# Kernel optimization log

Measured on AMD Instinct MI355X. Metric: run time of the kernel, lower is better.

## Reference

```python
import jax, jax.numpy as jnp
import numpy as np

# ---- static config (mirrors init_kwargs) ----
IN_CH = 64; COND_CH = 80; STRIDE = 8
DILATIONS = (1, 3, 9, 27); KS = 3; HOP = 256
HID = 64; KPKS = 3
B = 4; IN_LEN = 4096; COND_LEN = 128
N_LAYERS = len(DILATIONS)
OUT_CH = 2 * IN_CH
LW = IN_CH * OUT_CH * KS * N_LAYERS  # 98304
LB = OUT_CH * N_LAYERS               # 512


def leaky(x):
    return jax.nn.leaky_relu(x, 0.2)


def conv1d(x, w, b, dilation=1):
    # x: (B, T, Cin), w: (K, Cin, Cout) -> (B, T, Cout), 'same' padding
    y = jax.lax.conv_general_dilated(x, w, (1,), 'SAME', rhs_dilation=(dilation,),
                                     dimension_numbers=('NWC', 'WIO', 'NWC'))
    return y + b


def lvc(x, kernel, bias, hop):
    """Location-variable convolution, faithful to the TF extract_patches/reflect-pad
    implementation (call site uses dilation=1, kernel_size=3).
    x: (B, T, Cin); kernel: (B, L, Cin, Cout, K); bias: (B, L, Cout); T == L*hop."""
    Bn, T, C = x.shape
    K = kernel.shape[-1]
    p = (K - 1) // 2  # dilation = 1
    xp = jnp.pad(x, ((0, 0), (p, p), (0, 0)))
    L = T // hop
    # im2col: overlapping hop-segments of length hop+2p, stride hop -> (B, L, hop+2p, C)
    idx = jnp.arange(L)[:, None] * hop + jnp.arange(hop + 2 * p)[None, :]
    patches = xp[:, idx, :]
    patches = jnp.swapaxes(patches, 2, 3)  # (B, L, C, hop+2p)
    pad2 = hop - 1  # hop_size - dilation
    patches = jnp.pad(patches, ((0, 0), (0, 0), (0, 0), (pad2, pad2)), mode='reflect')
    patches = patches.reshape(Bn, L, C, -1, K)  # (B, L, C, hop, K) since 3*hop == hop*K
    out = jnp.einsum('blisk,bliok->blso', patches, kernel)  # (B, L, hop, Cout)
    out = out + bias[:, :, None, :]
    return out.reshape(Bn, T, -1)


def setup_inputs() -> dict:
    key = jax.random.key(0)
    ks = jax.random.split(key, 16)

    def w(k, shape):
        fan_in = float(np.prod(shape[:-1]))
        return (jax.random.normal(k, shape) / np.sqrt(fan_in)).astype(jnp.float32)

    return {
        'x': jax.random.normal(ks[0], (B, IN_LEN, IN_CH), jnp.float32),
        'c': jax.random.normal(ks[1], (B, COND_LEN, COND_CH), jnp.float32),
        # convt_pre transposed conv: (K=2*stride, Cin, Cout)
        'ct_w': w(ks[2], (2 * STRIDE, IN_CH, IN_CH)),
        'ct_b': jnp.zeros((IN_CH,), jnp.float32),
        # per-layer dilated convs (stacked over layers)
        'conv_w': w(ks[3], (N_LAYERS, KS, IN_CH, IN_CH)),
        'conv_b': jnp.zeros((N_LAYERS, IN_CH), jnp.float32),
        # kernel predictor: input conv
        'inp_w': w(ks[4], (5, COND_CH, HID)),
        'inp_b': jnp.zeros((HID,), jnp.float32),
        # 3 residual blocks, each with two convs
        'res_w1': w(ks[5], (3, KPKS, HID, HID)),
        'res_b1': jnp.zeros((3, HID), jnp.float32),
        'res_w2': w(ks[6], (3, KPKS, HID, HID)),
        'res_b2': jnp.zeros((3, HID), jnp.float32),
        # kernel / bias heads
        'kern_w': w(ks[7], (KPKS, HID, LW)),
        'kern_b': jnp.zeros((LW,), jnp.float32),
        'bias_w': w(ks[8], (KPKS, HID, LB)),
        'bias_b': jnp.zeros((LB,), jnp.float32),
    }


def reference(x, c, ct_w, ct_b, conv_w, conv_b, inp_w, inp_b,
              res_w1, res_b1, res_w2, res_b2, kern_w, kern_b, bias_w, bias_b):
    Bn = x.shape[0]
    # ---- convt_pre: LeakyReLU + ConvTranspose1d(stride, kernel=2*stride, 'same') ----
    h = leaky(x)
    h = jax.lax.conv_transpose(h, ct_w, strides=(STRIDE,), padding='SAME',
                               dimension_numbers=('NWC', 'WIO', 'NWC')) + ct_b
    # h: (B, IN_LEN*STRIDE, IN_CH)

    # ---- kernel predictor ----
    cc = leaky(conv1d(c, inp_w, inp_b))
    for j in range(3):
        t = leaky(conv1d(cc, res_w1[j], res_b1[j]))
        t = leaky(conv1d(t, res_w2[j], res_b2[j]))
        cc = cc + t
    k = conv1d(cc, kern_w, kern_b)   # (B, COND_LEN, LW)
    bb = conv1d(cc, bias_w, bias_b)  # (B, COND_LEN, LB)
    # faithful to TF: reshape (B, COND_LEN, LW) row-major into (B, layers, COND_LEN, ...)
    kernels = k.reshape(Bn, N_LAYERS, COND_LEN, IN_CH, OUT_CH, KS)
    biases = bb.reshape(Bn, N_LAYERS, COND_LEN, OUT_CH)

    # ---- LVC layers with sigmoid-tanh gating ----
    for i, d in enumerate(DILATIONS):
        out = leaky(conv1d(leaky(h), conv_w[i], conv_b[i], dilation=d))
        out = lvc(out, kernels[:, i], biases[:, i], HOP)  # (B, T, 2*IN_CH)
        h = h + jax.nn.sigmoid(out[..., :IN_CH]) * jnp.tanh(out[..., IN_CH:])
    return h
```

## Files before the change

### kernel.cpp

```cpp
#include <hip/hip_runtime.h>

#define TSZ 32768
#define LWN 98304

typedef float f32x4 __attribute__((ext_vector_type(4)));
typedef float f32x8 __attribute__((ext_vector_type(8)));
typedef short s16x8 __attribute__((ext_vector_type(8)));
typedef unsigned short u16x8 __attribute__((ext_vector_type(8)));

__device__ __forceinline__ float leaky(float x) { return x > 0.f ? x : 0.2f * x; }
__device__ __forceinline__ float bf2f(unsigned short b) { return __uint_as_float(((unsigned)b) << 16); }
__device__ __forceinline__ unsigned short f2bf(float f) {
  unsigned u = __float_as_uint(f);
  u += 0x7fffu + ((u >> 16) & 1u);
  return (unsigned short)(u >> 16);
}

__global__ __launch_bounds__(256) void ct_kernel(const float* __restrict__ x,
                                                 const float* __restrict__ ct_w,
                                                 const float* __restrict__ ct_b,
                                                 float* __restrict__ h) {
  __shared__ float wl[2 * 64 * 64];
  __shared__ float xl[17 * 64];
  int bid = blockIdx.x;
  int qc = bid & 255, phi = (bid >> 8) & 7, b = bid >> 11;
  int w0 = (11 - phi) & 7;
  int d0 = (phi + w0 - 11) >> 3;
  int tid = threadIdx.x;
  for (int e = tid; e < 8192; e += 256) {
    int w2 = e >> 12, rest = e & 4095;
    wl[e] = ct_w[(w0 + 8 * w2) * 4096 + rest];
  }
  int mstart = qc * 16 + d0;
  for (int e = tid; e < 17 * 64; e += 256) {
    int mr = e >> 6, i = e & 63;
    int m = mstart + mr;
    xl[e] = (m >= 0 && m < 4096) ? leaky(x[((b << 12) + m) * 64 + i]) : 0.f;
  }
  __syncthreads();
  int o = tid & 63, tg4 = tid >> 6;
  float bv = ct_b[o];
  float acc[4] = {bv, bv, bv, bv};
  for (int w2 = 0; w2 < 2; w2++) {
    const float* wp = &wl[w2 * 4096];
    int rbase = tg4 * 4 + w2;
    const float* xp = &xl[rbase * 64];
    for (int i = 0; i < 64; i++) {
      float wv = wp[i * 64 + o];
      acc[0] += xp[i] * wv;
      acc[1] += xp[64 + i] * wv;
      acc[2] += xp[128 + i] * wv;
      acc[3] += xp[192 + i] * wv;
    }
  }
  for (int r = 0; r < 4; r++) {
    int t = (qc * 16 + tg4 * 4 + r) * 8 + phi;
    h[(((size_t)b << 15) + t) * 64 + o] = acc[r];
  }
}

__global__ __launch_bounds__(256) void conv5_kernel(const float* __restrict__ c,
                                                    const float* __restrict__ w,
                                                    const float* __restrict__ bias,
                                                    float* __restrict__ cc) {
  int f = blockIdx.x * 256 + threadIdx.x;
  int o = f & 63, t = (f >> 6) & 127, b = f >> 13;
  float acc = bias[o];
  for (int kk = 0; kk < 5; kk++) {
    int tt = t + kk - 2;
    if (tt < 0 || tt >= 128) continue;
    const float* cr = c + (b * 128 + tt) * 80;
    const float* wr = w + kk * 80 * 64 + o;
    for (int i = 0; i < 80; i++) acc += cr[i] * wr[i * 64];
  }
  cc[f] = leaky(acc);
}

template <int ADD>
__global__ __launch_bounds__(256) void conv3_kernel(const float* __restrict__ xin,
                                                    const float* __restrict__ w,
                                                    const float* __restrict__ bias,
                                                    const float* __restrict__ addsrc,
                                                    float* __restrict__ out) {
  int f = blockIdx.x * 256 + threadIdx.x;
  int o = f & 63, t = (f >> 6) & 127, b = f >> 13;
  float acc = bias[o];
  for (int kk = 0; kk < 3; kk++) {
    int tt = t + kk - 1;
    if (tt < 0 || tt >= 128) continue;
    const float* xr = xin + (b * 128 + tt) * 64;
    const float* wr = w + kk * 64 * 64 + o;
    for (int i = 0; i < 64; i++) acc += xr[i] * wr[i * 64];
  }
  float v = leaky(acc);
  if (ADD) v += addsrc[f];
  out[f] = v;
}

__global__ __launch_bounds__(256) void patch_kernel(const float* __restrict__ cc,
                                                    float* __restrict__ A) {
  int f = blockIdx.x * 256 + threadIdx.x;
  int k = f % 192, m = f / 192;
  int b = m >> 7, l = m & 127;
  int kk = k >> 6, hh = k & 63;
  int ll = l + kk - 1;
  A[f] = (ll >= 0 && ll < 128) ? cc[((b << 7) + ll) * 64 + hh] : 0.f;
}

__global__ __launch_bounds__(256) void bbgemm_kernel(const float* __restrict__ A,
                                                     const float* __restrict__ w,
                                                     const float* __restrict__ bias,
                                                     float* __restrict__ bb) {
  int f = blockIdx.x * 256 + threadIdx.x;
  int n = f & 511, m = f >> 9;
  float acc = bias[n];
  const float* ar = A + m * 192;
  const float* wr = w + n;
  for (int k = 0; k < 192; k++) acc += ar[k] * wr[k * 512];
  bb[f] = acc;
}

__global__ __launch_bounds__(256) void wreorg_kernel(const float* __restrict__ W,
                                                     unsigned short* __restrict__ Wf) {
  int ft = blockIdx.x * 256 + threadIdx.x;
  int lane = ft & 63, fragid = ft >> 6;
  int kf = fragid % 6, nt = fragid / 6;
  int col = lane & 15, q = lane >> 4;
  int n = nt * 16 + col;
  u16x8 v;
  for (int j = 0; j < 8; j++) {
    int kki = kf * 32 + q * 8 + j;
    v[j] = f2bf(W[(size_t)kki * LWN + n]);
  }
  *(u16x8*)(Wf + ((size_t)fragid * 64 + lane) * 8) = v;
}

__global__ __launch_bounds__(256) void afrag_kernel(const float* __restrict__ A,
                                                    unsigned short* __restrict__ Af) {
  int ft = blockIdx.x * 256 + threadIdx.x;
  int lane = ft & 63, fragid = ft >> 6;
  int kf = fragid % 6, mt = fragid / 6;
  int row = lane & 15, q = lane >> 4;
  const float* ar = A + (mt * 16 + row) * 192 + kf * 32 + q * 8;
  u16x8 v;
  for (int j = 0; j < 8; j++) v[j] = f2bf(ar[j]);
  *(u16x8*)(Af + ((size_t)fragid * 64 + lane) * 8) = v;
}

__global__ __launch_bounds__(256) void dwfrag_kernel(const float* __restrict__ conv_w,
                                                     unsigned short* __restrict__ dwf) {
  int ft = blockIdx.x * 256 + threadIdx.x;
  int lane = ft & 63, frag = ft >> 6;
  int lay = frag / 24, fr = frag % 24;
  int nt = fr / 6, kf = fr % 6;
  int o = nt * 16 + (lane & 15);
  int k0 = kf * 32 + (lane >> 4) * 8;
  u16x8 v;
  for (int j = 0; j < 8; j++) {
    int k = k0 + j, kk = k >> 6, i = k & 63;
    v[j] = f2bf(conv_w[lay * 12288 + kk * 4096 + i * 64 + o]);
  }
  *(u16x8*)(dwf + ((size_t)frag * 64 + lane) * 8) = v;
}

__global__ __launch_bounds__(256) void kgemm_kernel(const unsigned short* __restrict__ Af,
                                                    const unsigned short* __restrict__ Wf,
                                                    const float* __restrict__ kern_b,
                                                    unsigned short* __restrict__ kbs) {
  int wave = threadIdx.x >> 6, lane = threadIdx.x & 63;
  int col = lane & 15, q = lane >> 4;
  int mt0 = blockIdx.y * 16 + wave * 4;
  int nt0 = blockIdx.x * 4;
  f32x4 acc[4][4];
  for (int a = 0; a < 4; a++)
    for (int cg = 0; cg < 4; cg++) acc[a][cg] = (f32x4){0.f, 0.f, 0.f, 0.f};
  const s16x8* ap = (const s16x8*)Af;
  const s16x8* bp = (const s16x8*)Wf;
  for (int kf = 0; kf < 6; kf++) {
    s16x8 av[4], bv[4];
    for (int a = 0; a < 4; a++) av[a] = ap[((mt0 + a) * 6 + kf) * 64 + lane];
    for (int cg = 0; cg < 4; cg++) bv[cg] = bp[((size_t)(nt0 + cg) * 6 + kf) * 64 + lane];
    for (int a = 0; a < 4; a++)
      for (int cg = 0; cg < 4; cg++)
        acc[a][cg] = __builtin_amdgcn_mfma_f32_16x16x32_bf16(av[a], bv[cg], acc[a][cg], 0, 0, 0);
  }
  for (int cg = 0; cg < 4; cg++) {
    int n = (nt0 + cg) * 16 + col;
    float bias = kern_b[n];
    for (int a = 0; a < 4; a++) {
      int mbase = (mt0 + a) * 16 + q * 4;
      for (int r = 0; r < 4; r++)
        kbs[(size_t)(mbase + r) * LWN + n] = f2bf(acc[a][cg][r] + bias);
    }
  }
}

__global__ __launch_bounds__(256) void dconv_kernel(const float* __restrict__ h,
                                                    const unsigned short* __restrict__ dwf,
                                                    const float* __restrict__ conv_b,
                                                    unsigned short* __restrict__ xc,
                                                    int lay, int d) {
  int tid = threadIdx.x;
  int w = tid >> 6, lane = tid & 63;
  int col = lane & 15, q = lane >> 4;
  int m0 = blockIdx.x * 256 + w * 64;
  int b = m0 >> 15, t0 = m0 & 32767;
  const float* hb = h + (((size_t)b) << 15) * 64;
  const s16x8* wf = (const s16x8*)(dwf + (size_t)lay * 24 * 512);

  f32x4 acc[4][4];
  for (int mt = 0; mt < 4; mt++)
    for (int cg = 0; cg < 4; cg++) acc[mt][cg] = (f32x4){0.f, 0.f, 0.f, 0.f};

#pragma unroll
  for (int kf = 0; kf < 6; kf++) {
    s16x8 bv[4];
#pragma unroll
    for (int cg = 0; cg < 4; cg++) bv[cg] = wf[(cg * 6 + kf) * 64 + lane];
    int k0 = kf * 32 + q * 8;
    int kk = k0 >> 6, i0 = k0 & 63;
    int dt = (kk - 1) * d;
    s16x8 ah[4], al[4];
#pragma unroll
    for (int mt = 0; mt < 4; mt++) {
      int t = t0 + mt * 16 + col + dt;
      bool oob = ((unsigned)t >= (unsigned)TSZ);
      int tc = oob ? 0 : t;
      f32x8 v = *(const f32x8*)(hb + (size_t)tc * 64 + i0);
#pragma unroll
      for (int j = 0; j < 8; j++) {
        float xv = oob ? 0.f : leaky(v[j]);
        unsigned short hi = f2bf(xv);
        ah[mt][j] = (short)hi;
        al[mt][j] = (short)f2bf(xv - bf2f(hi));
      }
    }
#pragma unroll
    for (int mt = 0; mt < 4; mt++)
#pragma unroll
      for (int cg = 0; cg < 4; cg++) {
        acc[mt][cg] = __builtin_amdgcn_mfma_f32_16x16x32_bf16(ah[mt], bv[cg], acc[mt][cg], 0, 0, 0);
        acc[mt][cg] = __builtin_amdgcn_mfma_f32_16x16x32_bf16(al[mt], bv[cg], acc[mt][cg], 0, 0, 0);
      }
  }

  unsigned short* xb = xc + (((size_t)b) << 15) * 64;
#pragma unroll
  for (int cg = 0; cg < 4; cg++) {
    int o = cg * 16 + col;
    float bias = conv_b[lay * 64 + o];
#pragma unroll
    for (int mt = 0; mt < 4; mt++)
#pragma unroll
      for (int r = 0; r < 4; r++) {
        int t = t0 + mt * 16 + q * 4 + r;
        xb[(size_t)t * 64 + o] = f2bf(leaky(acc[mt][cg][r] + bias));
      }
  }
}

__global__ __launch_bounds__(512) void lvc_kernel(const unsigned short* __restrict__ xc,
                                                  const unsigned short* __restrict__ kbs,
                                                  const float* __restrict__ bbv,
                                                  float* __restrict__ h, int lay) {
  int tid = threadIdx.x;
  int l = blockIdx.x & 127, b = blockIdx.x >> 7;
  int w = tid >> 6, lane = tid & 63;
  int wm = w & 3, wn = w >> 2;
  int col = lane & 15, qq = lane >> 4;
  const unsigned short* srow =
      kbs + (size_t)(b * 128 + lay * 32 + (l >> 2)) * LWN + (l & 3) * 24576;
  const unsigned short* xb = xc + (((size_t)b) << 15) * 64;

  f32x4 acc[4][4];
  for (int mt = 0; mt < 4; mt++)
    for (int cg = 0; cg < 4; cg++) acc[mt][cg] = (f32x4){0.f, 0.f, 0.f, 0.f};

  s16x8 av[2][4], bv[2][4];
  const s16x8 zfrag = {0, 0, 0, 0, 0, 0, 0, 0};

#define LOAD_STEP(p, kf)                                                            \
  {                                                                                 \
    int k0 = (kf) * 32 + qq * 8;                                                    \
    int kk = k0 >> 6, i0 = k0 & 63;                                                 \
    _Pragma("unroll") for (int mt = 0; mt < 4; mt++) {                              \
      int s = wm * 64 + mt * 16 + col;                                              \
      int nr = 3 * s + kk - 255;                                                    \
      int n = nr < 0 ? -nr : (nr >= 258 ? 514 - nr : nr);                           \
      int t = l * 256 + n - 1;                                                      \
      bool oob = ((unsigned)t >= (unsigned)TSZ);                                    \
      int tc = oob ? 0 : t;                                                         \
      s16x8 v = *(const s16x8*)(xb + (size_t)tc * 64 + i0);                         \
      av[p][mt] = oob ? zfrag : v;                                                  \
    }                                                                               \
    _Pragma("unroll") for (int cg = 0; cg < 4; cg++) {                              \
      int nt = 2 * wn + (cg & 1) + ((cg >> 1) << 2);                                \
      int o = nt * 16 + col;                                                        \
      const unsigned short* bp = srow + i0 * 384 + o * 3 + kk;                      \
      s16x8 bvv;                                                                    \
      _Pragma("unroll") for (int j = 0; j < 8; j++) bvv[j] = (short)bp[j * 384];    \
      bv[p][cg] = bvv;                                                              \
    }                                                                               \
  }

  LOAD_STEP(0, 0)
#pragma unroll
  for (int kf = 0; kf < 6; kf++) {
    int cur = kf & 1, nxt = cur ^ 1;
    if (kf < 5) LOAD_STEP(nxt, kf + 1)
#pragma unroll
    for (int mt = 0; mt < 4; mt++)
#pragma unroll
      for (int cg = 0; cg < 4; cg++)
        acc[mt][cg] =
            __builtin_amdgcn_mfma_f32_16x16x32_bf16(av[cur][mt], bv[cur][cg], acc[mt][cg], 0, 0, 0);
  }
#undef LOAD_STEP

  int lq = l >> 2, l2 = l & 3;
  const float* bb0 = bbv + (size_t)(b * 128 + lay * 32 + lq) * 512 + l2 * 128;
  float* hb = h + ((((size_t)b) << 15) + l * 256) * 64;
#pragma unroll
  for (int mt = 0; mt < 4; mt++) {
#pragma unroll
    for (int p = 0; p < 2; p++) {
      int o = (2 * wn + p) * 16 + col;
      float b0 = bb0[o], b1 = bb0[o + 64];
#pragma unroll
      for (int r = 0; r < 4; r++) {
        int s = wm * 64 + mt * 16 + qq * 4 + r;
        float a0 = acc[mt][p][r] + b0;
        float a1 = acc[mt][p + 2][r] + b1;
        float sg = 1.f / (1.f + __expf(-a0));
        float ex = __expf(2.f * a1);
        float th = 1.f - 2.f / (ex + 1.f);
        hb[(size_t)s * 64 + o] += sg * th;
      }
    }
  }
}

extern "C" void kernel_launch(void* const* d_in, const int* in_sizes, int n_in,
                              void* d_out, int out_size, void* d_ws, size_t ws_size,
                              hipStream_t stream) {
  (void)in_sizes; (void)n_in; (void)out_size; (void)ws_size;
  const float* x      = (const float*)d_in[0];
  const float* c      = (const float*)d_in[1];
  const float* ct_w   = (const float*)d_in[2];
  const float* ct_b   = (const float*)d_in[3];
  const float* conv_w = (const float*)d_in[4];
  const float* conv_b = (const float*)d_in[5];
  const float* inp_w  = (const float*)d_in[6];
  const float* inp_b  = (const float*)d_in[7];
  const float* res_w1 = (const float*)d_in[8];
  const float* res_b1 = (const float*)d_in[9];
  const float* res_w2 = (const float*)d_in[10];
  const float* res_b2 = (const float*)d_in[11];
  const float* kern_w = (const float*)d_in[12];
  const float* kern_b = (const float*)d_in[13];
  const float* bias_w = (const float*)d_in[14];
  const float* bias_b = (const float*)d_in[15];

  float* h = (float*)d_out;
  char* ws = (char*)d_ws;
  unsigned short* Wf = (unsigned short*)(ws);
  unsigned short* xc = (unsigned short*)(ws);
  unsigned short* kb = (unsigned short*)(ws + 37748736);
  float* A           = (float*)(ws + 138412032);
  unsigned short* Af = (unsigned short*)(ws + 138805248);
  float* cc          = (float*)(ws + 139001856);
  float* t1          = (float*)(ws + 139132928);
  float* bbv         = (float*)(ws + 139264000);
  unsigned short* dwf = (unsigned short*)(ws + 140312576);

  ct_kernel<<<dim3(8192), dim3(256), 0, stream>>>(x, ct_w, ct_b, h);
  conv5_kernel<<<dim3(128), dim3(256), 0, stream>>>(c, inp_w, inp_b, cc);
  for (int j = 0; j < 3; j++) {
    conv3_kernel<0><<<dim3(128), dim3(256), 0, stream>>>(cc, res_w1 + j * 12288, res_b1 + j * 64,
                                                         (const float*)nullptr, t1);
    conv3_kernel<1><<<dim3(128), dim3(256), 0, stream>>>(t1, res_w2 + j * 12288, res_b2 + j * 64,
                                                         cc, cc);
  }
  patch_kernel<<<dim3(384), dim3(256), 0, stream>>>(cc, A);
  bbgemm_kernel<<<dim3(1024), dim3(256), 0, stream>>>(A, bias_w, bias_b, bbv);
  wreorg_kernel<<<dim3(9216), dim3(256), 0, stream>>>(kern_w, Wf);
  afrag_kernel<<<dim3(48), dim3(256), 0, stream>>>(A, Af);
  kgemm_kernel<<<dim3(1536, 2), dim3(256), 0, stream>>>(Af, Wf, kern_b, kb);
  dwfrag_kernel<<<dim3(24), dim3(256), 0, stream>>>(conv_w, dwf);

  const int dil[4] = {1, 3, 9, 27};
  for (int lay = 0; lay < 4; lay++) {
    dconv_kernel<<<dim3(512), dim3(256), 0, stream>>>(h, dwf, conv_b, xc, lay, dil[lay]);
    lvc_kernel<<<dim3(512), dim3(512), 0, stream>>>(xc, kb, bbv, h, lay);
  }
}
```

Measured before the change: 637.6 us.

## Compute transposed convolution with split-bf16 MFMA instead of scalar FP32

Replaces the scalar FP32 shared-memory transposed-conv kernel with an MFMA-based GEMM. A small pre-kernel converts the weights into hi/lo bf16 fragments, and three bf16 MFMAs per tile emulate near-fp32 accuracy. Inputs get leaky applied and are split into hi/lo bf16 in registers, read directly from global memory. The aim is to cut the cost of the convt_pre stage, at the price of an extra launch and a small accuracy loss from dropping the lo*lo term.

```diff
diff --git a/kernel.cpp b/kernel.cpp
--- a/kernel.cpp
+++ b/kernel.cpp
@@ -16,46 +16,96 @@
   return (unsigned short)(u >> 16);
 }
 
-__global__ __launch_bounds__(256) void ct_kernel(const float* __restrict__ x,
-                                                 const float* __restrict__ ct_w,
-                                                 const float* __restrict__ ct_b,
-                                                 float* __restrict__ h) {
-  __shared__ float wl[2 * 64 * 64];
-  __shared__ float xl[17 * 64];
+__global__ __launch_bounds__(256) void ctwfrag_kernel(const float* __restrict__ ct_w,
+                                                      unsigned short* __restrict__ ctwf) {
+  int ft = blockIdx.x * 256 + threadIdx.x;
+  int lane = ft & 63, frag = ft >> 6;
+  int phi = frag >> 4, fr = frag & 15;
+  int nt = fr >> 2, kf = fr & 3;
+  int w0 = (11 - phi) & 7;
+  int o = nt * 16 + (lane & 15);
+  int k0 = kf * 32 + (lane >> 4) * 8;
+  u16x8 vh, vl;
+  for (int j = 0; j < 8; j++) {
+    int k = k0 + j, w2 = k >> 6, i = k & 63;
+    float wv = ct_w[(w0 + 8 * w2) * 4096 + i * 64 + o];
+    unsigned short hi = f2bf(wv);
+    vh[j] = hi;
+    vl[j] = f2bf(wv - bf2f(hi));
+  }
+  *(u16x8*)(ctwf + ((size_t)frag * 64 + lane) * 8) = vh;
+  *(u16x8*)(ctwf + ((size_t)(frag + 128) * 64 + lane) * 8) = vl;
+}
+
+__global__ __launch_bounds__(256) void ctm_kernel(const float* __restrict__ x,
+                                                  const unsigned short* __restrict__ ctwf,
+                                                  const float* __restrict__ ct_b,
+                                                  float* __restrict__ h) {
+  int tid = threadIdx.x;
+  int w = tid >> 6, lane = tid & 63;
+  int col = lane & 15, q = lane >> 4;
   int bid = blockIdx.x;
-  int qc = bid & 255, phi = (bid >> 8) & 7, b = bid >> 11;
+  int blk = bid & 15, phi = (bid >> 4) & 7, b = bid >> 7;
   int w0 = (11 - phi) & 7;
   int d0 = (phi + w0 - 11) >> 3;
-  int tid = threadIdx.x;
-  for (int e = tid; e < 8192; e += 256) {
-    int w2 = e >> 12, rest = e & 4095;
-    wl[e] = ct_w[(w0 + 8 * w2) * 4096 + rest];
-  }
-  int mstart = qc * 16 + d0;
-  for (int e = tid; e < 17 * 64; e += 256) {
-    int mr = e >> 6, i = e & 63;
-    int m = mstart + mr;
-    xl[e] = (m >= 0 && m < 4096) ? leaky(x[((b << 12) + m) * 64 + i]) : 0.f;
-  }
-  __syncthreads();
-  int o = tid & 63, tg4 = tid >> 6;
-  float bv = ct_b[o];
-  float acc[4] = {bv, bv, bv, bv};
-  for (int w2 = 0; w2 < 2; w2++) {
-    const float* wp = &wl[w2 * 4096];
-    int rbase = tg4 * 4 + w2;
-    const float* xp = &xl[rbase * 64];
-    for (int i = 0; i < 64; i++) {
-      float wv = wp[i * 64 + o];
-      acc[0] += xp[i] * wv;
-      acc[1] += xp[64 + i] * wv;
-      acc[2] += xp[128 + i] * wv;
-      acc[3] += xp[192 + i] * wv;
+  int mm0 = blk * 256 + w * 64;
+  const float* xb = x + (((size_t)b) << 12) * 64;
+  const s16x8* wf = (const s16x8*)ctwf;
+
+  f32x4 acc[4][4];
+  for (int mt = 0; mt < 4; mt++)
+    for (int cg = 0; cg < 4; cg++) acc[mt][cg] = (f32x4){0.f, 0.f, 0.f, 0.f};
+
+#pragma unroll
+  for (int kf = 0; kf < 4; kf++) {
+    s16x8 bh[4], bl[4];
+#pragma unroll
+    for (int cg = 0; cg < 4; cg++) {
+      int frag = (phi * 4 + cg) * 4 + kf;
+      bh[cg] = wf[frag * 64 + lane];
+      bl[cg] = wf[(frag + 128) * 64 + lane];
     }
-  }
-  for (int r = 0; r < 4; r++) {
-    int t = (qc * 16 + tg4 * 4 + r) * 8 + phi;
-    h[(((size_t)b << 15) + t) * 64 + o] = acc[r];
+    int k0 = kf * 32 + q * 8;
+    int w2 = k0 >> 6, i0 = k0 & 63;
+    int rb = mm0 + d0 + w2;
+    s16x8 ah[4], al[4];
+#pragma unroll
+    for (int mt = 0; mt < 4; mt++) {
+      int r = rb + mt * 16 + col;
+      bool oob = ((unsigned)r >= 4096u);
+      int rc = oob ? 0 : r;
+      f32x8 v = *(const f32x8*)(xb + (size_t)rc * 64 + i0);
+#pragma unroll
+      for (int j = 0; j < 8; j++) {
+        float xv = oob ? 0.f : leaky(v[j]);
+        unsigned short hi = f2bf(xv);
+        ah[mt][j] = (short)hi;
+        al[mt][j] = (short)f2bf(xv - bf2f(hi));
+      }
+    }
+#pragma unroll
+    for (int mt = 0; mt < 4; mt++)
+#pragma unroll
+      for (int cg = 0; cg < 4; cg++) {
+        acc[mt][cg] = __builtin_amdgcn_mfma_f32_16x16x32_bf16(ah[mt], bh[cg], acc[mt][cg], 0, 0, 0);
+        acc[mt][cg] = __builtin_amdgcn_mfma_f32_16x16x32_bf16(al[mt], bh[cg], acc[mt][cg], 0, 0, 0);
+        acc[mt][cg] = __builtin_amdgcn_mfma_f32_16x16x32_bf16(ah[mt], bl[cg], acc[mt][cg], 0, 0, 0);
+      }
+  }
+
+  float* hb = h + (((size_t)b) << 15) * 64;
+#pragma unroll
+  for (int cg = 0; cg < 4; cg++) {
+    int o = cg * 16 + col;
+    float bias = ct_b[o];
+#pragma unroll
+    for (int mt = 0; mt < 4; mt++)
+#pragma unroll
+      for (int r = 0; r < 4; r++) {
+        int mm = mm0 + mt * 16 + q * 4 + r;
+        int t = mm * 8 + phi;
+        hb[(size_t)t * 64 + o] = acc[mt][cg][r] + bias;
+      }
   }
 }
 
@@ -372,8 +422,10 @@
   float* t1          = (float*)(ws + 139132928);
   float* bbv         = (float*)(ws + 139264000);
   unsigned short* dwf = (unsigned short*)(ws + 140312576);
-
-  ct_kernel<<<dim3(8192), dim3(256), 0, stream>>>(x, ct_w, ct_b, h);
+  unsigned short* ctwf = (unsigned short*)(ws + 138412032);
+
+  ctwfrag_kernel<<<dim3(32), dim3(256), 0, stream>>>(ct_w, ctwf);
+  ctm_kernel<<<dim3(512), dim3(256), 0, stream>>>(x, ctwf, ct_b, h);
   conv5_kernel<<<dim3(128), dim3(256), 0, stream>>>(c, inp_w, inp_b, cc);
   for (int j = 0; j < 3; j++) {
     conv3_kernel<0><<<dim3(128), dim3(256), 0, stream>>>(cc, res_w1 + j * 12288, res_b1 + j * 64,
```

Result: faster. 565.2 us (-11.4%).
